# Optimization experiments

Hardware: AMD Instinct MI355X
Metric: run time of the kernel (lower is better)

## Reference

```python
import jax, jax.numpy as jnp
import numpy as np

EMBED_DIM = 1024
NUM_HEADS = 16
HEAD_DIM = EMBED_DIM // NUM_HEADS


def setup_inputs() -> dict:
    key = jax.random.key(0)
    ks = jax.random.split(key, 5)
    B, N, C = 4, 2048, EMBED_DIM
    x = jax.random.normal(ks[0], (B, N, C), dtype=jnp.float32)
    # Linear params (PyTorch layout: weight [out, in])
    s = 1.0 / np.sqrt(C)
    W_qkv = jax.random.uniform(ks[1], (3 * C, C), dtype=jnp.float32, minval=-s, maxval=s)
    b_qkv = jax.random.uniform(ks[2], (3 * C,), dtype=jnp.float32, minval=-s, maxval=s)
    W_out = jax.random.uniform(ks[3], (C, C), dtype=jnp.float32, minval=-s, maxval=s)
    b_out = jax.random.uniform(ks[4], (C,), dtype=jnp.float32, minval=-s, maxval=s)
    return {"x": x, "W_qkv": W_qkv, "b_qkv": b_qkv, "W_out": W_out, "b_out": b_out}


def _rotate_half(t):
    t1, t2 = jnp.split(t, 2, axis=-1)
    return jnp.concatenate((-t2, t1), axis=-1)


def _rope_cos_sin(seq_len, dim, dtype):
    inv_freq = 1.0 / (10000.0 ** (jnp.arange(0, dim, 2, dtype=jnp.float32) / dim))
    t = jnp.arange(seq_len, dtype=jnp.float32)
    freqs = jnp.einsum("i,j->ij", t, inv_freq)  # [N, dim/2]
    emb = jnp.concatenate((freqs, freqs), axis=-1)  # [N, dim]
    return emb.astype(dtype)


def reference(x, W_qkv, b_qkv, W_out, b_out):
    B, N, C = x.shape
    H, D = NUM_HEADS, HEAD_DIM
    qkv = x @ W_qkv.T + b_qkv  # [B, N, 3C]
    qkv = qkv.reshape(B, N, 3, H, D).transpose(2, 0, 3, 1, 4)  # [3, B, H, N, D]
    q, k, v = qkv[0], qkv[1], qkv[2]
    emb = _rope_cos_sin(N, D, x.dtype)
    cos = jnp.cos(emb)[None, None, :, :]  # [1,1,N,D]
    sin = jnp.sin(emb)[None, None, :, :]
    q = q * cos + _rotate_half(q) * sin
    k = k * cos + _rotate_half(k) * sin
    scale = D ** -0.5
    attn = jnp.einsum("bhnd,bhmd->bhnm", q, k) * scale  # [B,H,N,N]
    attn = jax.nn.softmax(attn, axis=-1)
    out = jnp.einsum("bhnm,bhmd->bhnd", attn, v)  # [B,H,N,D]
    out = out.transpose(0, 2, 1, 3).reshape(B, N, C)
    return out @ W_out.T + b_out
```

## Files before the change

kernel.cpp:

```cpp
#include <hip/hip_runtime.h>
#include <hip/hip_bf16.h>
#include <cstdint>
#include <cstddef>

#define SEQ 2048
#define NBATCH 4
#define EMB 1024
#define NH 16
#define HD 64
#define MTOT (NBATCH * SEQ)

typedef __attribute__((ext_vector_type(8))) short bf16x8;
typedef __attribute__((ext_vector_type(4))) float f32x4;
typedef __attribute__((ext_vector_type(16))) float f32x16;
typedef unsigned short u16;
typedef unsigned int u32;

__device__ __forceinline__ float bf2f(u16 v) {
  union { u32 u; float f; } c; c.u = ((u32)v) << 16; return c.f;
}
__device__ __forceinline__ u16 f2bf(float f) {
  union { float f; u32 u; } c; c.f = f;
  u32 u = c.u;
  return (u16)((u + 0x7FFFu + ((u >> 16) & 1u)) >> 16);
}
__device__ __forceinline__ u32 f2u(float f) {
  union { float f; u32 u; } c; c.f = f; return c.u;
}

__global__ void cast_kernel(const float* __restrict__ in, u16* __restrict__ out, int n4) {
  int stride = gridDim.x * blockDim.x;
  for (int i = blockIdx.x * blockDim.x + threadIdx.x; i < n4; i += stride) {
    float4 v = reinterpret_cast<const float4*>(in)[i];
    ushort4 o;
    o.x = f2bf(v.x); o.y = f2bf(v.y); o.z = f2bf(v.z); o.w = f2bf(v.w);
    reinterpret_cast<ushort4*>(out)[i] = o;
  }
}

__global__ void rope_table_kernel(float* __restrict__ tab) {
  int i = blockIdx.x * blockDim.x + threadIdx.x;
  if (i >= SEQ * 32) return;
  int n = i >> 5, j = i & 31;
  float invf = 1.0f / powf(10000.0f, (float)(2 * j) / 64.0f);
  float ang = (float)n * invf;
  tab[i] = cosf(ang);
  tab[SEQ * 32 + i] = sinf(ang);
}

__device__ __forceinline__ void gld_lds16(const u16* g, u16* l) {
  __builtin_amdgcn_global_load_lds((const __attribute__((address_space(1))) void*)g,
                                   (__attribute__((address_space(3))) void*)l, 16, 0, 0);
}

template<bool OUT_F32>
__global__ __launch_bounds__(256, 2)
void gemm_bt(const u16* __restrict__ A, const u16* __restrict__ Bw,
             const float* __restrict__ bias, void* __restrict__ Cout,
             int N, int tiles_n) {
  __shared__ u16 lA[128 * 64];
  __shared__ u16 lB[128 * 64];
  const int K = 1024;
  int bm = blockIdx.x / tiles_n;
  int bn = blockIdx.x % tiles_n;
  int t = threadIdx.x;
  int wave = t >> 6, lane = t & 63;
  int wm = wave >> 1, wn = wave & 1;
  int l15 = lane & 15, l4 = lane >> 4;

  f32x4 acc[4][4];
#pragma unroll
  for (int i = 0; i < 4; ++i)
#pragma unroll
    for (int j = 0; j < 4; ++j) acc[i][j] = (f32x4){0.f, 0.f, 0.f, 0.f};

  int su[4], sr[4], sc[4];
#pragma unroll
  for (int i = 0; i < 4; ++i) {
    int u = (i * 4 + wave) * 64 + lane;
    su[i] = u;
    sr[i] = u >> 3;
    sc[i] = (u & 7) ^ (sr[i] & 7);
  }

  for (int kt = 0; kt < K / 64; ++kt) {
    if (kt) __syncthreads();
#pragma unroll
    for (int i = 0; i < 4; ++i) {
      gld_lds16(A + (size_t)(bm * 128 + sr[i]) * K + kt * 64 + sc[i] * 8, &lA[su[i] * 8]);
      gld_lds16(Bw + (size_t)(bn * 128 + sr[i]) * K + kt * 64 + sc[i] * 8, &lB[su[i] * 8]);
    }
    __syncthreads();
#pragma unroll
    for (int ks = 0; ks < 2; ++ks) {
      bf16x8 af[4], bfr[4];
#pragma unroll
      for (int mb = 0; mb < 4; ++mb) {
        int r = wm * 64 + mb * 16 + l15;
        int cc = (ks * 4 + l4) ^ (r & 7);
        af[mb] = *reinterpret_cast<const bf16x8*>(&lA[r * 64 + cc * 8]);
      }
#pragma unroll
      for (int nb = 0; nb < 4; ++nb) {
        int r = wn * 64 + nb * 16 + l15;
        int cc = (ks * 4 + l4) ^ (r & 7);
        bfr[nb] = *reinterpret_cast<const bf16x8*>(&lB[r * 64 + cc * 8]);
      }
#pragma unroll
      for (int mb = 0; mb < 4; ++mb)
#pragma unroll
        for (int nb = 0; nb < 4; ++nb)
          acc[mb][nb] = __builtin_amdgcn_mfma_f32_16x16x32_bf16(af[mb], bfr[nb], acc[mb][nb], 0, 0, 0);
    }
  }

#pragma unroll
  for (int mb = 0; mb < 4; ++mb)
#pragma unroll
    for (int nb = 0; nb < 4; ++nb) {
      int row0 = bm * 128 + wm * 64 + mb * 16 + l4 * 4;
      int col = bn * 128 + wn * 64 + nb * 16 + l15;
      float bv = bias[col];
#pragma unroll
      for (int r = 0; r < 4; ++r) {
        float v = acc[mb][nb][r] + bv;
        if (OUT_F32)
          reinterpret_cast<float*>(Cout)[(size_t)(row0 + r) * N + col] = v;
        else
          reinterpret_cast<u16*>(Cout)[(size_t)(row0 + r) * N + col] = f2bf(v);
      }
    }
}

__global__ __launch_bounds__(256)
void rope_scatter(const u16* __restrict__ qkv, const float* __restrict__ tab,
                  u16* __restrict__ Q, u16* __restrict__ Kk, u16* __restrict__ Vt) {
  int blk = blockIdx.x;
  int bh = blk >> 5;
  int nt = blk & 31;
  int b = bh >> 4, h = bh & 15;
  int t = threadIdx.x;
  __shared__ u16 vtile[64][72];
  const float* ct = tab;
  const float* st = tab + SEQ * 32;
#pragma unroll
  for (int p = 0; p < 2; ++p) {
    int u = p * 256 + t;
    int r = u >> 3, g = u & 7;
    int n = nt * 64 + r;
    size_t base = (size_t)(b * SEQ + n) * 3072;
    int d0 = g * 8;
    int f0 = d0 & 31;
    bf16x8 qv = *reinterpret_cast<const bf16x8*>(&qkv[base + h * 64 + d0]);
    bf16x8 qp = *reinterpret_cast<const bf16x8*>(&qkv[base + h * 64 + (d0 ^ 32)]);
    bf16x8 kv = *reinterpret_cast<const bf16x8*>(&qkv[base + 1024 + h * 64 + d0]);
    bf16x8 kp = *reinterpret_cast<const bf16x8*>(&qkv[base + 1024 + h * 64 + (d0 ^ 32)]);
    bf16x8 vv = *reinterpret_cast<const bf16x8*>(&qkv[base + 2048 + h * 64 + d0]);
    float4 c0 = *reinterpret_cast<const float4*>(&ct[n * 32 + f0]);
    float4 c1 = *reinterpret_cast<const float4*>(&ct[n * 32 + f0 + 4]);
    float4 s0 = *reinterpret_cast<const float4*>(&st[n * 32 + f0]);
    float4 s1 = *reinterpret_cast<const float4*>(&st[n * 32 + f0 + 4]);
    float sgn = (d0 < 32) ? -1.0f : 1.0f;
    float cs[8] = {c0.x, c0.y, c0.z, c0.w, c1.x, c1.y, c1.z, c1.w};
    float sn[8] = {s0.x, s0.y, s0.z, s0.w, s1.x, s1.y, s1.z, s1.w};
    bf16x8 qo, ko;
#pragma unroll
    for (int j = 0; j < 8; ++j) {
      float qr = bf2f((u16)qv[j]) * cs[j] + sgn * bf2f((u16)qp[j]) * sn[j];
      float kr = bf2f((u16)kv[j]) * cs[j] + sgn * bf2f((u16)kp[j]) * sn[j];
      qo[j] = (short)f2bf(qr * 0.1803368801111163f);
      ko[j] = (short)f2bf(kr);
      vtile[d0 + j][r] = (u16)vv[j];
    }
    size_t qbase = ((size_t)bh * SEQ + n) * 64 + d0;
    *reinterpret_cast<bf16x8*>(&Q[qbase]) = qo;
    *reinterpret_cast<bf16x8*>(&Kk[qbase]) = ko;
  }
  __syncthreads();
#pragma unroll
  for (int p = 0; p < 2; ++p) {
    int u = p * 256 + t;
    int d = u >> 3, c = u & 7;
    bf16x8 o = *reinterpret_cast<const bf16x8*>(&vtile[d][c * 8]);
    *reinterpret_cast<bf16x8*>(&Vt[((size_t)bh * 64 + d) * SEQ + nt * 64 + c * 8]) = o;
  }
}

__global__ __launch_bounds__(256, 4)
void attn_kernel(const u16* __restrict__ Q, const u16* __restrict__ Kk,
                 const u16* __restrict__ Vt, u16* __restrict__ Out) {
  int bid = blockIdx.x;
  int swz = (bid & 7) * 128 + (bid >> 3);
  int bh = swz >> 4;
  int qt = swz & 15;
  int b = bh >> 4, h = bh & 15;
  int t = threadIdx.x;
  int wave = t >> 6, lane = t & 63;
  int l31 = lane & 31, hi = lane >> 5;

  __shared__ u16 lK[2][64 * 64];
  __shared__ u16 lV[2][64 * 64];

  const u16* Qh = Q + (size_t)bh * SEQ * 64;
  const u16* Kh = Kk + (size_t)bh * SEQ * 64;
  const u16* Vh = Vt + (size_t)bh * 64 * SEQ;
  int q0w = qt * 128 + wave * 32;

  bf16x8 qf[4];
#pragma unroll
  for (int dc = 0; dc < 4; ++dc)
    qf[dc] = *reinterpret_cast<const bf16x8*>(
        &Qh[(size_t)(q0w + l31) * 64 + dc * 16 + hi * 8]);

  f32x16 oacc[2];
#pragma unroll
  for (int db = 0; db < 2; ++db)
#pragma unroll
    for (int r = 0; r < 16; ++r) oacc[db][r] = 0.f;
  float dn = 0.f;

  auto stage = [&](int buf, int kt) {
#pragma unroll
    for (int p = 0; p < 2; ++p) {
      int u = p * 256 + t;
      int r = u >> 3;
      int c = (u & 7) ^ (r & 7);
      gld_lds16(Kh + (size_t)(kt * 64 + r) * 64 + c * 8, &lK[buf][u * 8]);
      gld_lds16(Vh + (size_t)r * SEQ + kt * 64 + c * 8, &lV[buf][u * 8]);
    }
  };

  union PF { u32 w[4]; bf16x8 v; };
  int cur = 0;
  stage(0, 0);
  for (int kt = 0; kt < SEQ / 64; ++kt) {
    if (kt + 1 < SEQ / 64) {
      stage(cur ^ 1, kt + 1);
      asm volatile("s_waitcnt vmcnt(4)" ::: "memory");
    } else {
      asm volatile("s_waitcnt vmcnt(0)" ::: "memory");
    }
    __builtin_amdgcn_s_barrier();

    f32x16 s[2];
#pragma unroll
    for (int cb = 0; cb < 2; ++cb)
#pragma unroll
      for (int r = 0; r < 16; ++r) s[cb][r] = 0.f;
    __builtin_amdgcn_s_setprio(1);
#pragma unroll
    for (int cb = 0; cb < 2; ++cb) {
      int krow = cb * 32 + l31;
#pragma unroll
      for (int dc = 0; dc < 4; ++dc) {
        int ch = (dc * 2 + hi) ^ (l31 & 7);
        bf16x8 kf = *reinterpret_cast<const bf16x8*>(&lK[cur][krow * 64 + ch * 8]);
        s[cb] = __builtin_amdgcn_mfma_f32_32x32x16_bf16(kf, qf[dc], s[cb], 0, 0, 0);
      }
    }
    __builtin_amdgcn_s_setprio(0);

    PF pa[2][2];
#pragma unroll
    for (int cb = 0; cb < 2; ++cb) {
#pragma unroll
      for (int r = 0; r < 16; ++r) {
        float e = __builtin_amdgcn_exp2f(s[cb][r]);
        s[cb][r] = e;
        dn += e;
      }
#pragma unroll
      for (int c = 0; c < 2; ++c) {
        u32 u0 = f2u(s[cb][8 * c + 0]) + 0x8000u;
        u32 u1 = f2u(s[cb][8 * c + 1]) + 0x8000u;
        u32 u2 = f2u(s[cb][8 * c + 2]) + 0x8000u;
        u32 u3 = f2u(s[cb][8 * c + 3]) + 0x8000u;
        u32 u4 = f2u(s[cb][8 * c + 4]) + 0x8000u;
        u32 u5 = f2u(s[cb][8 * c + 5]) + 0x8000u;
        u32 u6 = f2u(s[cb][8 * c + 6]) + 0x8000u;
        u32 u7 = f2u(s[cb][8 * c + 7]) + 0x8000u;
        u32 a1 = __builtin_amdgcn_perm(u1, u0, 0x07060302);
        u32 a2 = __builtin_amdgcn_perm(u3, u2, 0x07060302);
        u32 b1 = __builtin_amdgcn_perm(u5, u4, 0x07060302);
        u32 b2 = __builtin_amdgcn_perm(u7, u6, 0x07060302);
        asm("v_permlane32_swap_b32 %0, %1" : "+v"(a1), "+v"(b1));
        asm("v_permlane32_swap_b32 %0, %1" : "+v"(a2), "+v"(b2));
        pa[cb][c].w[0] = a1; pa[cb][c].w[1] = a2;
        pa[cb][c].w[2] = b1; pa[cb][c].w[3] = b2;
      }
    }

    __builtin_amdgcn_s_setprio(1);
#pragma unroll
    for (int cb = 0; cb < 2; ++cb)
#pragma unroll
      for (int c = 0; c < 2; ++c)
#pragma unroll
        for (int db = 0; db < 2; ++db) {
          int vrow = db * 32 + l31;
          int ch = (cb * 4 + c * 2 + hi) ^ (l31 & 7);
          bf16x8 vf = *reinterpret_cast<const bf16x8*>(&lV[cur][vrow * 64 + ch * 8]);
          oacc[db] = __builtin_amdgcn_mfma_f32_32x32x16_bf16(pa[cb][c].v, vf, oacc[db], 0, 0, 0);
        }
    __builtin_amdgcn_s_setprio(0);
    __builtin_amdgcn_s_barrier();
    cur ^= 1;
  }

  dn += __shfl_xor(dn, 32);
#pragma unroll
  for (int r = 0; r < 16; ++r) {
    int qrel = (r & 3) + 8 * (r >> 2) + 4 * hi;
    float dfull = __shfl(dn, qrel);
    float inv = __builtin_amdgcn_rcpf(dfull);
    int q = q0w + qrel;
#pragma unroll
    for (int db = 0; db < 2; ++db) {
      int d = db * 32 + l31;
      Out[(size_t)(b * SEQ + q) * EMB + h * 64 + d] = f2bf(oacc[db][r] * inv);
    }
  }
}

extern "C" void kernel_launch(void* const* d_in, const int* in_sizes, int n_in,
                              void* d_out, int out_size, void* d_ws, size_t ws_size,
                              hipStream_t stream) {
  const float* x = (const float*)d_in[0];
  const float* bqkv = (const float*)d_in[2];
  const float* bout = (const float*)d_in[4];
  float* out = (float*)d_out;

  char* ws = (char*)d_ws;
  size_t off = 0;
  auto alloc = [&](size_t bytes) {
    void* p = ws + off;
    off += (bytes + 255) & ~(size_t)255;
    return p;
  };
  u16* xb    = (u16*)alloc((size_t)MTOT * EMB * 2);
  u16* wqkvb = (u16*)alloc((size_t)3 * EMB * EMB * 2);
  u16* woutb = (u16*)alloc((size_t)EMB * EMB * 2);
  u16* qkv   = (u16*)alloc((size_t)MTOT * 3 * EMB * 2);
  u16* Qb    = (u16*)alloc((size_t)64 * SEQ * HD * 2);
  u16* Kb    = (u16*)alloc((size_t)64 * SEQ * HD * 2);
  u16* Vtb   = (u16*)alloc((size_t)64 * HD * SEQ * 2);
  u16* aout  = (u16*)alloc((size_t)MTOT * EMB * 2);
  float* tab = (float*)alloc((size_t)2 * SEQ * 32 * 4);
  (void)ws_size; (void)in_sizes; (void)n_in; (void)out_size;

  cast_kernel<<<2048, 256, 0, stream>>>(x, xb, MTOT * EMB / 4);
  cast_kernel<<<1024, 256, 0, stream>>>((const float*)d_in[1], wqkvb, 3 * EMB * EMB / 4);
  cast_kernel<<<512, 256, 0, stream>>>((const float*)d_in[3], woutb, EMB * EMB / 4);
  rope_table_kernel<<<(SEQ * 32 + 255) / 256, 256, 0, stream>>>(tab);

  gemm_bt<false><<<64 * 24, 256, 0, stream>>>(xb, wqkvb, bqkv, qkv, 3 * EMB, 24);
  rope_scatter<<<64 * 32, 256, 0, stream>>>(qkv, tab, Qb, Kb, Vtb);
  attn_kernel<<<64 * 16, 256, 0, stream>>>(Qb, Kb, Vtb, aout);
  gemm_bt<true><<<64 * 8, 256, 0, stream>>>(aout, woutb, bout, out, EMB, 8);
}
```

Measured before the change: 199.5 us.

## Fuse RoPE and Q/K/V scatter into QKV GEMM epilogue, drop LDS swizzle

Moves RoPE rotation, Q scaling and the head-major Q/K/transposed-V scatter into the QKV GEMM epilogue. This removes the intermediate qkv buffer and the separate rope_scatter kernel, saving a full write and read of the QKV activations. The cos/sin table is interleaved so each lane reads one float2 per pair. The attention kernel's LDS layout is changed from XOR-swizzled rows to a chunk-major layout. In exchange, the epilogue stores become narrow 2-byte scattered writes (and strided ushort4 for V), and the new LDS layout may change bank-conflict behaviour.

```diff
diff --git a/kernel.cpp b/kernel.cpp
--- a/kernel.cpp
+++ b/kernel.cpp
@@ -38,14 +38,14 @@
   }
 }
 
-__global__ void rope_table_kernel(float* __restrict__ tab) {
+__global__ void rope_table2_kernel(float* __restrict__ tab2) {
   int i = blockIdx.x * blockDim.x + threadIdx.x;
   if (i >= SEQ * 32) return;
   int n = i >> 5, j = i & 31;
   float invf = 1.0f / powf(10000.0f, (float)(2 * j) / 64.0f);
   float ang = (float)n * invf;
-  tab[i] = cosf(ang);
-  tab[SEQ * 32 + i] = sinf(ang);
+  tab2[2 * i] = cosf(ang);
+  tab2[2 * i + 1] = sinf(ang);
 }
 
 __device__ __forceinline__ void gld_lds16(const u16* g, u16* l) {
@@ -53,11 +53,10 @@
                                    (__attribute__((address_space(3))) void*)l, 16, 0, 0);
 }
 
-template<bool OUT_F32>
 __global__ __launch_bounds__(256, 2)
-void gemm_bt(const u16* __restrict__ A, const u16* __restrict__ Bw,
-             const float* __restrict__ bias, void* __restrict__ Cout,
-             int N, int tiles_n) {
+void gemm_bt_f32(const u16* __restrict__ A, const u16* __restrict__ Bw,
+                 const float* __restrict__ bias, float* __restrict__ Cout,
+                 int N, int tiles_n) {
   __shared__ u16 lA[128 * 64];
   __shared__ u16 lB[128 * 64];
   const int K = 1024;
@@ -122,67 +121,122 @@
       int col = bn * 128 + wn * 64 + nb * 16 + l15;
       float bv = bias[col];
 #pragma unroll
+      for (int r = 0; r < 4; ++r)
+        Cout[(size_t)(row0 + r) * N + col] = acc[mb][nb][r] + bv;
+    }
+}
+
+__global__ __launch_bounds__(256, 2)
+void gemm_qkv_rope(const u16* __restrict__ A, const u16* __restrict__ Bw,
+                   const float* __restrict__ bias, const float* __restrict__ tab2,
+                   u16* __restrict__ Qb, u16* __restrict__ Kb, u16* __restrict__ Vtb) {
+  __shared__ u16 lA[128 * 64];
+  __shared__ u16 lB[128 * 64];
+  const int K = 1024, tiles_n = 24;
+  int bm = blockIdx.x / tiles_n;
+  int bn = blockIdx.x % tiles_n;
+  int t = threadIdx.x;
+  int wave = t >> 6, lane = t & 63;
+  int wm = wave >> 1, wn = wave & 1;
+  int l15 = lane & 15, l4 = lane >> 4;
+
+  f32x4 acc[4][4];
+#pragma unroll
+  for (int i = 0; i < 4; ++i)
+#pragma unroll
+    for (int j = 0; j < 4; ++j) acc[i][j] = (f32x4){0.f, 0.f, 0.f, 0.f};
+
+  int su[4], sr[4], sc[4];
+#pragma unroll
+  for (int i = 0; i < 4; ++i) {
+    int u = (i * 4 + wave) * 64 + lane;
+    su[i] = u;
+    sr[i] = u >> 3;
+    sc[i] = (u & 7) ^ (sr[i] & 7);
+  }
+
+  for (int kt = 0; kt < K / 64; ++kt) {
+    if (kt) __syncthreads();
+#pragma unroll
+    for (int i = 0; i < 4; ++i) {
+      gld_lds16(A + (size_t)(bm * 128 + sr[i]) * K + kt * 64 + sc[i] * 8, &lA[su[i] * 8]);
+      gld_lds16(Bw + (size_t)(bn * 128 + sr[i]) * K + kt * 64 + sc[i] * 8, &lB[su[i] * 8]);
+    }
+    __syncthreads();
+#pragma unroll
+    for (int ks = 0; ks < 2; ++ks) {
+      bf16x8 af[4], bfr[4];
+#pragma unroll
+      for (int mb = 0; mb < 4; ++mb) {
+        int r = wm * 64 + mb * 16 + l15;
+        int cc = (ks * 4 + l4) ^ (r & 7);
+        af[mb] = *reinterpret_cast<const bf16x8*>(&lA[r * 64 + cc * 8]);
+      }
+#pragma unroll
+      for (int nb = 0; nb < 4; ++nb) {
+        int r = wn * 64 + nb * 16 + l15;
+        int cc = (ks * 4 + l4) ^ (r & 7);
+        bfr[nb] = *reinterpret_cast<const bf16x8*>(&lB[r * 64 + cc * 8]);
+      }
+#pragma unroll
+      for (int mb = 0; mb < 4; ++mb)
+#pragma unroll
+        for (int nb = 0; nb < 4; ++nb)
+          acc[mb][nb] = __builtin_amdgcn_mfma_f32_16x16x32_bf16(af[mb], bfr[nb], acc[mb][nb], 0, 0, 0);
+    }
+  }
+
+  int type = bn >> 3;
+  int h = (bn * 2 + wn) & 15;
+  int colbase = bn * 128 + wn * 64;
+  float bv[4];
+#pragma unroll
+  for (int nb = 0; nb < 4; ++nb) bv[nb] = bias[colbase + nb * 16 + l15];
+
+  if (type < 2) {
+    u16* dst0 = (type == 0) ? Qb : Kb;
+    float qs = (type == 0) ? 0.1803368801111163f : 1.0f;
+#pragma unroll
+    for (int mb = 0; mb < 4; ++mb) {
+      int row0 = bm * 128 + wm * 64 + mb * 16 + l4 * 4;
+#pragma unroll
       for (int r = 0; r < 4; ++r) {
-        float v = acc[mb][nb][r] + bv;
-        if (OUT_F32)
-          reinterpret_cast<float*>(Cout)[(size_t)(row0 + r) * N + col] = v;
-        else
-          reinterpret_cast<u16*>(Cout)[(size_t)(row0 + r) * N + col] = f2bf(v);
-      }
-    }
-}
-
-__global__ __launch_bounds__(256)
-void rope_scatter(const u16* __restrict__ qkv, const float* __restrict__ tab,
-                  u16* __restrict__ Q, u16* __restrict__ Kk, u16* __restrict__ Vt) {
-  int blk = blockIdx.x;
-  int bh = blk >> 5;
-  int nt = blk & 31;
-  int b = bh >> 4, h = bh & 15;
-  int t = threadIdx.x;
-  __shared__ u16 vtile[64][72];
-  const float* ct = tab;
-  const float* st = tab + SEQ * 32;
-#pragma unroll
-  for (int p = 0; p < 2; ++p) {
-    int u = p * 256 + t;
-    int r = u >> 3, g = u & 7;
-    int n = nt * 64 + r;
-    size_t base = (size_t)(b * SEQ + n) * 3072;
-    int d0 = g * 8;
-    int f0 = d0 & 31;
-    bf16x8 qv = *reinterpret_cast<const bf16x8*>(&qkv[base + h * 64 + d0]);
-    bf16x8 qp = *reinterpret_cast<const bf16x8*>(&qkv[base + h * 64 + (d0 ^ 32)]);
-    bf16x8 kv = *reinterpret_cast<const bf16x8*>(&qkv[base + 1024 + h * 64 + d0]);
-    bf16x8 kp = *reinterpret_cast<const bf16x8*>(&qkv[base + 1024 + h * 64 + (d0 ^ 32)]);
-    bf16x8 vv = *reinterpret_cast<const bf16x8*>(&qkv[base + 2048 + h * 64 + d0]);
-    float4 c0 = *reinterpret_cast<const float4*>(&ct[n * 32 + f0]);
-    float4 c1 = *reinterpret_cast<const float4*>(&ct[n * 32 + f0 + 4]);
-    float4 s0 = *reinterpret_cast<const float4*>(&st[n * 32 + f0]);
-    float4 s1 = *reinterpret_cast<const float4*>(&st[n * 32 + f0 + 4]);
-    float sgn = (d0 < 32) ? -1.0f : 1.0f;
-    float cs[8] = {c0.x, c0.y, c0.z, c0.w, c1.x, c1.y, c1.z, c1.w};
-    float sn[8] = {s0.x, s0.y, s0.z, s0.w, s1.x, s1.y, s1.z, s1.w};
-    bf16x8 qo, ko;
-#pragma unroll
-    for (int j = 0; j < 8; ++j) {
-      float qr = bf2f((u16)qv[j]) * cs[j] + sgn * bf2f((u16)qp[j]) * sn[j];
-      float kr = bf2f((u16)kv[j]) * cs[j] + sgn * bf2f((u16)kp[j]) * sn[j];
-      qo[j] = (short)f2bf(qr * 0.1803368801111163f);
-      ko[j] = (short)f2bf(kr);
-      vtile[d0 + j][r] = (u16)vv[j];
-    }
-    size_t qbase = ((size_t)bh * SEQ + n) * 64 + d0;
-    *reinterpret_cast<bf16x8*>(&Q[qbase]) = qo;
-    *reinterpret_cast<bf16x8*>(&Kk[qbase]) = ko;
-  }
-  __syncthreads();
-#pragma unroll
-  for (int p = 0; p < 2; ++p) {
-    int u = p * 256 + t;
-    int d = u >> 3, c = u & 7;
-    bf16x8 o = *reinterpret_cast<const bf16x8*>(&vtile[d][c * 8]);
-    *reinterpret_cast<bf16x8*>(&Vt[((size_t)bh * 64 + d) * SEQ + nt * 64 + c * 8]) = o;
+        int row = row0 + r;
+        int bb = row >> 11, nl = row & 2047;
+        const float* tp = tab2 + (size_t)nl * 64;
+        float2 cs  = *reinterpret_cast<const float2*>(tp + 2 * l15);
+        float2 cs2 = *reinterpret_cast<const float2*>(tp + 2 * (16 + l15));
+        float a0 = acc[mb][0][r] + bv[0];
+        float a1 = acc[mb][1][r] + bv[1];
+        float a2 = acc[mb][2][r] + bv[2];
+        float a3 = acc[mb][3][r] + bv[3];
+        float o0 = (a0 * cs.x  - a2 * cs.y)  * qs;
+        float o2 = (a2 * cs.x  + a0 * cs.y)  * qs;
+        float o1 = (a1 * cs2.x - a3 * cs2.y) * qs;
+        float o3 = (a3 * cs2.x + a1 * cs2.y) * qs;
+        u16* dst = dst0 + ((size_t)(bb * 16 + h) * SEQ + nl) * 64;
+        dst[l15]      = f2bf(o0);
+        dst[16 + l15] = f2bf(o1);
+        dst[32 + l15] = f2bf(o2);
+        dst[48 + l15] = f2bf(o3);
+      }
+    }
+  } else {
+#pragma unroll
+    for (int mb = 0; mb < 4; ++mb) {
+      int row0 = bm * 128 + wm * 64 + mb * 16 + l4 * 4;
+      int bb = row0 >> 11, nl0 = row0 & 2047;
+#pragma unroll
+      for (int nb = 0; nb < 4; ++nb) {
+        int d = nb * 16 + l15;
+        ushort4 pk;
+        pk.x = f2bf(acc[mb][nb][0] + bv[nb]);
+        pk.y = f2bf(acc[mb][nb][1] + bv[nb]);
+        pk.z = f2bf(acc[mb][nb][2] + bv[nb]);
+        pk.w = f2bf(acc[mb][nb][3] + bv[nb]);
+        *reinterpret_cast<ushort4*>(&Vtb[((size_t)(bb * 16 + h) * 64 + d) * SEQ + nl0]) = pk;
+      }
+    }
   }
 }
 
@@ -198,8 +252,8 @@
   int wave = t >> 6, lane = t & 63;
   int l31 = lane & 31, hi = lane >> 5;
 
-  __shared__ u16 lK[2][64 * 64];
-  __shared__ u16 lV[2][64 * 64];
+  __shared__ u16 lK[2][512 * 8];
+  __shared__ u16 lV[2][512 * 8];
 
   const u16* Qh = Q + (size_t)bh * SEQ * 64;
   const u16* Kh = Kk + (size_t)bh * SEQ * 64;
@@ -223,10 +277,8 @@
 #pragma unroll
     for (int p = 0; p < 2; ++p) {
       int u = p * 256 + t;
-      int r = u >> 3;
-      int c = (u & 7) ^ (r & 7);
-      gld_lds16(Kh + (size_t)(kt * 64 + r) * 64 + c * 8, &lK[buf][u * 8]);
-      gld_lds16(Vh + (size_t)r * SEQ + kt * 64 + c * 8, &lV[buf][u * 8]);
+      gld_lds16(Kh + (size_t)(kt * 64 + (u & 63)) * 64 + (u >> 6) * 8, &lK[buf][u * 8]);
+      gld_lds16(Vh + (size_t)(u & 63) * SEQ + kt * 64 + (u >> 6) * 8, &lV[buf][u * 8]);
     }
   };
 
@@ -250,11 +302,10 @@
     __builtin_amdgcn_s_setprio(1);
 #pragma unroll
     for (int cb = 0; cb < 2; ++cb) {
-      int krow = cb * 32 + l31;
 #pragma unroll
       for (int dc = 0; dc < 4; ++dc) {
-        int ch = (dc * 2 + hi) ^ (l31 & 7);
-        bf16x8 kf = *reinterpret_cast<const bf16x8*>(&lK[cur][krow * 64 + ch * 8]);
+        bf16x8 kf = *reinterpret_cast<const bf16x8*>(
+            &lK[cur][(((dc * 2 + hi) << 6) + cb * 32 + l31) * 8]);
         s[cb] = __builtin_amdgcn_mfma_f32_32x32x16_bf16(kf, qf[dc], s[cb], 0, 0, 0);
       }
     }
@@ -297,9 +348,8 @@
       for (int c = 0; c < 2; ++c)
 #pragma unroll
         for (int db = 0; db < 2; ++db) {
-          int vrow = db * 32 + l31;
-          int ch = (cb * 4 + c * 2 + hi) ^ (l31 & 7);
-          bf16x8 vf = *reinterpret_cast<const bf16x8*>(&lV[cur][vrow * 64 + ch * 8]);
+          bf16x8 vf = *reinterpret_cast<const bf16x8*>(
+              &lV[cur][(((cb * 4 + c * 2 + hi) << 6) + db * 32 + l31) * 8]);
           oacc[db] = __builtin_amdgcn_mfma_f32_32x32x16_bf16(pa[cb][c].v, vf, oacc[db], 0, 0, 0);
         }
     __builtin_amdgcn_s_setprio(0);
@@ -340,21 +390,19 @@
   u16* xb    = (u16*)alloc((size_t)MTOT * EMB * 2);
   u16* wqkvb = (u16*)alloc((size_t)3 * EMB * EMB * 2);
   u16* woutb = (u16*)alloc((size_t)EMB * EMB * 2);
-  u16* qkv   = (u16*)alloc((size_t)MTOT * 3 * EMB * 2);
   u16* Qb    = (u16*)alloc((size_t)64 * SEQ * HD * 2);
   u16* Kb    = (u16*)alloc((size_t)64 * SEQ * HD * 2);
   u16* Vtb   = (u16*)alloc((size_t)64 * HD * SEQ * 2);
   u16* aout  = (u16*)alloc((size_t)MTOT * EMB * 2);
-  float* tab = (float*)alloc((size_t)2 * SEQ * 32 * 4);
+  float* tab2 = (float*)alloc((size_t)SEQ * 32 * 2 * 4);
   (void)ws_size; (void)in_sizes; (void)n_in; (void)out_size;
 
   cast_kernel<<<2048, 256, 0, stream>>>(x, xb, MTOT * EMB / 4);
   cast_kernel<<<1024, 256, 0, stream>>>((const float*)d_in[1], wqkvb, 3 * EMB * EMB / 4);
   cast_kernel<<<512, 256, 0, stream>>>((const float*)d_in[3], woutb, EMB * EMB / 4);
-  rope_table_kernel<<<(SEQ * 32 + 255) / 256, 256, 0, stream>>>(tab);
-
-  gemm_bt<false><<<64 * 24, 256, 0, stream>>>(xb, wqkvb, bqkv, qkv, 3 * EMB, 24);
-  rope_scatter<<<64 * 32, 256, 0, stream>>>(qkv, tab, Qb, Kb, Vtb);
+  rope_table2_kernel<<<(SEQ * 32 + 255) / 256, 256, 0, stream>>>(tab2);
+
+  gemm_qkv_rope<<<64 * 24, 256, 0, stream>>>(xb, wqkvb, bqkv, tab2, Qb, Kb, Vtb);
   attn_kernel<<<64 * 16, 256, 0, stream>>>(Qb, Kb, Vtb, aout);
-  gemm_bt<true><<<64 * 8, 256, 0, stream>>>(aout, woutb, bout, out, EMB, 8);
-}
+  gemm_bt_f32<<<64 * 8, 256, 0, stream>>>(aout, woutb, bout, out, EMB, 8);
+}
```

Measured after the change: 194.1 us. -2.7%, faster.
